# Optimization experiments

Measured on AMD Instinct MI355X. Metric: run time of the kernel, lower is better.

The kernel has to match this reference:

```python
import jax, jax.numpy as jnp
import numpy as np

N_NODES = 100000
N_EDGES = 1600000
IN_C = 128
OUT_C = 64
EDGE_DIM = 32
BN_EPS = 1e-5


def setup_inputs() -> dict:
    key = jax.random.key(0)
    ks = jax.random.split(key, 10)
    s = lambda fan_in: 1.0 / np.sqrt(fan_in)
    return {
        "x": jax.random.normal(ks[0], (N_NODES, IN_C), jnp.float32),
        "edge_index": jax.random.randint(ks[1], (2, N_EDGES), 0, N_NODES, jnp.int64),
        "edge_attr": jax.random.normal(ks[2], (N_EDGES, EDGE_DIM), jnp.float32),
        # SAGEConv params: lin_l (neighbors, with bias), lin_r (root, no bias)
        "W_l": jax.random.uniform(ks[3], (IN_C, OUT_C), jnp.float32, -s(IN_C), s(IN_C)),
        "b_l": jnp.zeros((OUT_C,), jnp.float32),
        "W_r": jax.random.uniform(ks[4], (IN_C, OUT_C), jnp.float32, -s(IN_C), s(IN_C)),
        # edge_transform: Linear(EDGE_DIM, OUT_C)
        "W_e": jax.random.uniform(ks[5], (EDGE_DIM, OUT_C), jnp.float32, -s(EDGE_DIM), s(EDGE_DIM)),
        "b_e": jax.random.uniform(ks[6], (OUT_C,), jnp.float32, -s(EDGE_DIM), s(EDGE_DIM)),
        # gate: Linear(2*OUT_C, OUT_C)
        "W_g": jax.random.uniform(ks[7], (2 * OUT_C, OUT_C), jnp.float32, -s(2 * OUT_C), s(2 * OUT_C)),
        "b_g": jax.random.uniform(ks[8], (OUT_C,), jnp.float32, -s(2 * OUT_C), s(2 * OUT_C)),
        # BatchNorm1d affine params
        "gamma": jnp.ones((OUT_C,), jnp.float32),
        "beta": jnp.zeros((OUT_C,), jnp.float32),
    }


def reference(x, edge_index, edge_attr, W_l, b_l, W_r, W_e, b_e, W_g, b_g, gamma, beta):
    n = x.shape[0]
    row, col = edge_index[0], edge_index[1]  # source, target

    # --- SAGEConv (mean aggregation): agg[i] = mean_{e: col[e]==i} x[row[e]]
    agg = jax.ops.segment_sum(x[row], col, num_segments=n)  # [N, IN_C]
    cnt = jax.ops.segment_sum(jnp.ones((row.shape[0],), x.dtype), col, num_segments=n)
    agg = agg / jnp.maximum(cnt, 1.0)[:, None]
    out = agg @ W_l + b_l + x @ W_r  # [N, OUT_C]

    # --- edge gating
    ea = edge_attr @ W_e + b_e  # [E, OUT_C]
    combined = jnp.concatenate([out[col], ea], axis=-1)  # [E, 2*OUT_C]
    gate = jax.nn.sigmoid(combined @ W_g + b_g)  # [E, OUT_C]
    contrib = gate * ea  # [E, OUT_C]
    out = out + jax.ops.segment_sum(contrib, col, num_segments=n)

    # --- BatchNorm1d (training: batch stats, biased variance)
    mu = jnp.mean(out, axis=0)
    var = jnp.mean(jnp.square(out - mu), axis=0)
    out = gamma * (out - mu) * jax.lax.rsqrt(var + BN_EPS) + beta

    # residual = Identity -> out + out, then ReLU
    return jax.nn.relu(2.0 * out)
```

## Files before the change

kernel.cpp:

```cpp
#include <hip/hip_runtime.h>
#include <math.h>

#define NN 100000
#define NE 1600000
#define INC 128
#define OC 64
#define ED 32

typedef __attribute__((ext_vector_type(8))) short bf16x8;
typedef __attribute__((ext_vector_type(4))) float f32x4;

__device__ __forceinline__ float sigmoidf_(float z) {
    return __builtin_amdgcn_rcpf(1.0f + __expf(-z));
}

__device__ __forceinline__ unsigned short f2bf(float x) {
    unsigned int u = __float_as_uint(x);
    unsigned int r = u + 0x7FFFu + ((u >> 16) & 1u);
    return (unsigned short)(r >> 16);
}
__device__ __forceinline__ float bf2f(unsigned short u) {
    return __uint_as_float((unsigned int)u << 16);
}
__device__ __forceinline__ unsigned cvtpk(float lo, float hi) {
    unsigned r;
    asm("v_cvt_pk_bf16_f32 %0, %1, %2" : "=v"(r) : "v"(lo), "v"(hi));
    return r;
}

extern "C" __global__ void __launch_bounds__(256)
k_wfuse(const float* __restrict__ We, const float* __restrict__ be,
        const float* __restrict__ Wg, const float* __restrict__ Wl,
        const float* __restrict__ Wr, unsigned short* __restrict__ WfT,
        unsigned short* __restrict__ WeT, float* __restrict__ hb,
        unsigned short* __restrict__ WlrT) {
    int idx = blockIdx.x * 256 + threadIdx.x;
    if (idx < ED * OC) {
        int ch = idx >> 5, d = idx & 31;
        float acc = 0.0f;
#pragma unroll
        for (int k = 0; k < OC; ++k)
            acc = fmaf(We[d * OC + k], Wg[(OC + k) * OC + ch], acc);
        WfT[idx] = f2bf(acc);
    } else if (idx < 2 * ED * OC) {
        int i2 = idx - ED * OC;
        int ch = i2 >> 5, d = i2 & 31;
        WeT[i2] = f2bf(We[d * OC + ch]);
    } else if (idx < 2 * ED * OC + OC) {
        int j = idx - 2 * ED * OC;
        float acc = 0.0f;
#pragma unroll
        for (int k = 0; k < OC; ++k)
            acc = fmaf(be[k], Wg[(OC + k) * OC + j], acc);
        hb[j] = acc;
    } else if (idx < 2 * ED * OC + OC + 2 * INC * OC) {
        int i3 = idx - (2 * ED * OC + OC);
        int ch = i3 >> 7, k = i3 & 127;
        float v = (ch < OC) ? Wl[k * OC + ch] : Wr[k * OC + (ch - OC)];
        WlrT[i3] = f2bf(v);
    }
}

extern "C" __global__ void __launch_bounds__(256)
k_xw(const float* __restrict__ x, const unsigned short* __restrict__ WlrT,
     unsigned short* __restrict__ ybf, unsigned short* __restrict__ xwrbf) {
    __shared__ unsigned short xs[64][136];
    int t = threadIdx.x;
    int base = blockIdx.x * 64;
    {
        int rr = t >> 2, cc = (t & 3) * 32;
        int grow = base + rr;
        if (grow < NN) {
            const float4* xp = reinterpret_cast<const float4*>(
                x + (size_t)grow * INC + cc);
#pragma unroll
            for (int q = 0; q < 8; ++q) {
                float4 v = xp[q];
                uint2 uv;
                uv.x = cvtpk(v.x, v.y);
                uv.y = cvtpk(v.z, v.w);
                *reinterpret_cast<uint2*>(&xs[rr][cc + q * 4]) = uv;
            }
        } else {
#pragma unroll
            for (int q = 0; q < 8; ++q) {
                uint2 uv; uv.x = 0u; uv.y = 0u;
                *reinterpret_cast<uint2*>(&xs[rr][cc + q * 4]) = uv;
            }
        }
    }
    __syncthreads();

    int lane = t & 63, w = t >> 6;
    int c = lane & 15, g = lane >> 4;

    bf16x8 bw0[4], bw1[4];
#pragma unroll
    for (int kk = 0; kk < 4; ++kk) {
        bw0[kk] = *reinterpret_cast<const bf16x8*>(
            WlrT + (w * 32 + 0 * 16 + c) * INC + kk * 32 + g * 8);
        bw1[kk] = *reinterpret_cast<const bf16x8*>(
            WlrT + (w * 32 + 1 * 16 + c) * INC + kk * 32 + g * 8);
    }

    f32x4 acc[4][2];
#pragma unroll
    for (int mt = 0; mt < 4; ++mt)
#pragma unroll
        for (int nt = 0; nt < 2; ++nt)
            acc[mt][nt] = (f32x4){0.0f, 0.0f, 0.0f, 0.0f};

#pragma unroll
    for (int kk = 0; kk < 4; ++kk) {
        bf16x8 a0 = *reinterpret_cast<const bf16x8*>(&xs[0 * 16 + c][kk * 32 + g * 8]);
        bf16x8 a1 = *reinterpret_cast<const bf16x8*>(&xs[1 * 16 + c][kk * 32 + g * 8]);
        bf16x8 a2 = *reinterpret_cast<const bf16x8*>(&xs[2 * 16 + c][kk * 32 + g * 8]);
        bf16x8 a3 = *reinterpret_cast<const bf16x8*>(&xs[3 * 16 + c][kk * 32 + g * 8]);
        acc[0][0] = __builtin_amdgcn_mfma_f32_16x16x32_bf16(a0, bw0[kk], acc[0][0], 0, 0, 0);
        acc[0][1] = __builtin_amdgcn_mfma_f32_16x16x32_bf16(a0, bw1[kk], acc[0][1], 0, 0, 0);
        acc[1][0] = __builtin_amdgcn_mfma_f32_16x16x32_bf16(a1, bw0[kk], acc[1][0], 0, 0, 0);
        acc[1][1] = __builtin_amdgcn_mfma_f32_16x16x32_bf16(a1, bw1[kk], acc[1][1], 0, 0, 0);
        acc[2][0] = __builtin_amdgcn_mfma_f32_16x16x32_bf16(a2, bw0[kk], acc[2][0], 0, 0, 0);
        acc[2][1] = __builtin_amdgcn_mfma_f32_16x16x32_bf16(a2, bw1[kk], acc[2][1], 0, 0, 0);
        acc[3][0] = __builtin_amdgcn_mfma_f32_16x16x32_bf16(a3, bw0[kk], acc[3][0], 0, 0, 0);
        acc[3][1] = __builtin_amdgcn_mfma_f32_16x16x32_bf16(a3, bw1[kk], acc[3][1], 0, 0, 0);
    }

#pragma unroll
    for (int mt = 0; mt < 4; ++mt) {
#pragma unroll
        for (int nt = 0; nt < 2; ++nt) {
            int ch = w * 32 + nt * 16 + c;
#pragma unroll
            for (int j = 0; j < 4; ++j) {
                int row = base + mt * 16 + g * 4 + j;
                if (row < NN) {
                    unsigned short vb = f2bf(acc[mt][nt][j]);
                    if (ch < OC) ybf[(size_t)row * OC + ch] = vb;
                    else         xwrbf[(size_t)row * OC + (ch - OC)] = vb;
                }
            }
        }
    }
}

extern "C" __global__ void __launch_bounds__(256)
k_hist(const int* __restrict__ colv, int* __restrict__ cnti) {
    int e = blockIdx.x * 256 + threadIdx.x;
    if (e >= NE) return;
    int cl = colv[e];
    cl = min(max(cl, 0), NN - 1);
    atomicAdd(&cnti[cl], 1);
}

extern "C" __global__ void __launch_bounds__(1024)
k_scanA(const int* __restrict__ cnti, int* __restrict__ cur,
        int* __restrict__ bsum) {
    __shared__ int s[1024];
    int t = threadIdx.x;
    int idx = blockIdx.x * 1024 + t;
    int v = (idx < NN) ? cnti[idx] : 0;
    s[t] = v;
    __syncthreads();
#pragma unroll
    for (int off = 1; off < 1024; off <<= 1) {
        int tmp = (t >= off) ? s[t - off] : 0;
        __syncthreads();
        s[t] += tmp;
        __syncthreads();
    }
    if (idx < NN) cur[idx] = s[t] - v;
    if (t == 1023) bsum[blockIdx.x] = s[1023];
}

extern "C" __global__ void __launch_bounds__(128)
k_scanB(int* __restrict__ bsum) {
    __shared__ int s[128];
    int t = threadIdx.x;
    int v = (t < 98) ? bsum[t] : 0;
    s[t] = v;
    __syncthreads();
#pragma unroll
    for (int off = 1; off < 128; off <<= 1) {
        int tmp = (t >= off) ? s[t - off] : 0;
        __syncthreads();
        s[t] += tmp;
        __syncthreads();
    }
    if (t < 98) bsum[t] = s[t] - v;
}

extern "C" __global__ void __launch_bounds__(1024)
k_scanC(int* __restrict__ cur, const int* __restrict__ bsum) {
    int idx = blockIdx.x * 1024 + threadIdx.x;
    if (idx < NN) cur[idx] += bsum[blockIdx.x];
}

extern "C" __global__ void __launch_bounds__(256)
k_bucket(const int* __restrict__ colv, const int* __restrict__ rowv,
         int* __restrict__ cur, unsigned long long* __restrict__ ec) {
    int e = blockIdx.x * 256 + threadIdx.x;
    if (e >= NE) return;
    int cl = colv[e];
    cl = min(max(cl, 0), NN - 1);
    int r = rowv[e];
    r = min(max(r, 0), NN - 1);
    int pos = atomicAdd(&cur[cl], 1);
    ec[pos] = ((unsigned long long)(unsigned)r << 47) |
              ((unsigned long long)(unsigned)cl << 30) | (unsigned)e;
}

extern "C" __global__ void __launch_bounds__(256)
k_aggoh(const unsigned long long* __restrict__ ec, const int* __restrict__ cur,
        const unsigned short* __restrict__ ybf, unsigned short* xwr_h,
        const float* __restrict__ bl, const float* __restrict__ Wg,
        const float* __restrict__ bg, const float* __restrict__ hb,
        float* __restrict__ agg) {
    __shared__ float ol[4][64];
    int w = threadIdx.x >> 6, c = threadIdx.x & 63;
    int i = blockIdx.x * 4 + w;
    if (i >= NN) return;
    int start = (i == 0) ? 0 : cur[i - 1];
    int end = cur[i];
    float xwr = bf2f(xwr_h[(size_t)i * OC + c]);
    float acc = 0.0f;
    int p = start;
    for (; p + 3 < end; p += 4) {
        int r0 = (int)(ec[p + 0] >> 47);
        int r1 = (int)(ec[p + 1] >> 47);
        int r2 = (int)(ec[p + 2] >> 47);
        int r3 = (int)(ec[p + 3] >> 47);
        unsigned short u0 = ybf[(size_t)r0 * OC + c];
        unsigned short u1 = ybf[(size_t)r1 * OC + c];
        unsigned short u2 = ybf[(size_t)r2 * OC + c];
        unsigned short u3 = ybf[(size_t)r3 * OC + c];
        acc += bf2f(u0);
        acc += bf2f(u1);
        acc += bf2f(u2);
        acc += bf2f(u3);
    }
    for (; p < end; ++p) {
        int r0 = (int)(ec[p] >> 47);
        acc += bf2f(ybf[(size_t)r0 * OC + c]);
    }
    float inv = 1.0f / fmaxf((float)(end - start), 1.0f);
    float o = fmaf(acc, inv, bl[c] + xwr);
    agg[(size_t)i * OC + c] = o;
    ol[w][c] = o;
    __builtin_amdgcn_wave_barrier();
    float h0 = bg[c] + hb[c];
    float h1 = 0.0f, h2 = 0.0f, h3 = 0.0f;
#pragma unroll
    for (int k = 0; k < OC; k += 4) {
        float o0 = ol[w][k + 0], o1 = ol[w][k + 1];
        float o2 = ol[w][k + 2], o3 = ol[w][k + 3];
        h0 = fmaf(o0, Wg[(k + 0) * OC + c], h0);
        h1 = fmaf(o1, Wg[(k + 1) * OC + c], h1);
        h2 = fmaf(o2, Wg[(k + 2) * OC + c], h2);
        h3 = fmaf(o3, Wg[(k + 3) * OC + c], h3);
    }
    float h = (h0 + h1) + (h2 + h3);
    xwr_h[(size_t)i * OC + (c & 15) * 4 + (c >> 4)] = f2bf(h);
}

extern "C" __global__ void __launch_bounds__(256, 3)
k_gate_ns(const unsigned long long* __restrict__ ec, const float* __restrict__ eattr,
          const unsigned short* __restrict__ WfT, const unsigned short* __restrict__ WeT,
          const float* __restrict__ be, const unsigned short* __restrict__ hswz,
          unsigned short* __restrict__ contrib) {
    int lane = threadIdx.x & 63;
    int w = threadIdx.x >> 6;
    int tb = (blockIdx.x * 4 + w) * 64;

    unsigned long long ev = ec[tb + lane];
    int e = (int)(ev & 0x3FFFFFFFULL);
    int cl = (int)((ev >> 30) & 0x1FFFFULL);
    int c = lane & 15, g = lane >> 4;

    int erow0 = __shfl(e, 0 * 16 + c);
    int erow1 = __shfl(e, 1 * 16 + c);
    int erow2 = __shfl(e, 2 * 16 + c);
    int erow3 = __shfl(e, 3 * 16 + c);
    int clx[16];
#pragma unroll
    for (int mt = 0; mt < 4; ++mt)
#pragma unroll
        for (int r = 0; r < 4; ++r)
            clx[mt * 4 + r] = __shfl(cl, mt * 16 + g * 4 + r);

    uint2 hg[16];
#pragma unroll
    for (int q = 0; q < 16; ++q)
        hg[q] = *reinterpret_cast<const uint2*>(hswz + (size_t)clx[q] * OC + c * 4);

    bf16x8 bwf[4], bwe[4];
    float bev[4];
#pragma unroll
    for (int nt = 0; nt < 4; ++nt) {
        int ch = nt * 16 + c;
        bwf[nt] = *reinterpret_cast<const bf16x8*>(WfT + ch * ED + g * 8);
        bwe[nt] = *reinterpret_cast<const bf16x8*>(WeT + ch * ED + g * 8);
        bev[nt] = be[ch];
    }

    float4 alo0 = reinterpret_cast<const float4*>(eattr + (size_t)erow0 * ED + g * 8)[0];
    float4 ahi0 = reinterpret_cast<const float4*>(eattr + (size_t)erow0 * ED + g * 8)[1];
    float4 alo1 = reinterpret_cast<const float4*>(eattr + (size_t)erow1 * ED + g * 8)[0];
    float4 ahi1 = reinterpret_cast<const float4*>(eattr + (size_t)erow1 * ED + g * 8)[1];
    float4 alo2 = reinterpret_cast<const float4*>(eattr + (size_t)erow2 * ED + g * 8)[0];
    float4 ahi2 = reinterpret_cast<const float4*>(eattr + (size_t)erow2 * ED + g * 8)[1];
    float4 alo3 = reinterpret_cast<const float4*>(eattr + (size_t)erow3 * ED + g * 8)[0];
    float4 ahi3 = reinterpret_cast<const float4*>(eattr + (size_t)erow3 * ED + g * 8)[1];

    bf16x8 afr[4];
    {
        union { bf16x8 v; unsigned d[4]; } pk;
#define PACKA(idx, lo, hi)                         \
        pk.d[0] = cvtpk(lo.x, lo.y);               \
        pk.d[1] = cvtpk(lo.z, lo.w);               \
        pk.d[2] = cvtpk(hi.x, hi.y);               \
        pk.d[3] = cvtpk(hi.z, hi.w);               \
        afr[idx] = pk.v;
        PACKA(0, alo0, ahi0)
        PACKA(1, alo1, ahi1)
        PACKA(2, alo2, ahi2)
        PACKA(3, alo3, ahi3)
#undef PACKA
    }

#pragma unroll
    for (int mt = 0; mt < 4; ++mt) {
        uint2 h0 = hg[mt * 4 + 0];
        uint2 h1 = hg[mt * 4 + 1];
        uint2 h2 = hg[mt * 4 + 2];
        uint2 h3 = hg[mt * 4 + 3];
        float sv[4][4];
#pragma unroll
        for (int nt = 0; nt < 4; ++nt) {
            f32x4 cz, ce;
            unsigned w0 = (nt < 2) ? h0.x : h0.y;
            unsigned w1 = (nt < 2) ? h1.x : h1.y;
            unsigned w2 = (nt < 2) ? h2.x : h2.y;
            unsigned w3 = (nt < 2) ? h3.x : h3.y;
            cz[0] = bf2f((unsigned short)((nt & 1) ? (w0 >> 16) : (w0 & 0xffffu)));
            cz[1] = bf2f((unsigned short)((nt & 1) ? (w1 >> 16) : (w1 & 0xffffu)));
            cz[2] = bf2f((unsigned short)((nt & 1) ? (w2 >> 16) : (w2 & 0xffffu)));
            cz[3] = bf2f((unsigned short)((nt & 1) ? (w3 >> 16) : (w3 & 0xffffu)));
            ce[0] = bev[nt]; ce[1] = bev[nt]; ce[2] = bev[nt]; ce[3] = bev[nt];
            f32x4 z  = __builtin_amdgcn_mfma_f32_16x16x32_bf16(afr[mt], bwf[nt], cz, 0, 0, 0);
            f32x4 ea = __builtin_amdgcn_mfma_f32_16x16x32_bf16(afr[mt], bwe[nt], ce, 0, 0, 0);
            sv[nt][0] = sigmoidf_(z[0]) * ea[0];
            sv[nt][1] = sigmoidf_(z[1]) * ea[1];
            sv[nt][2] = sigmoidf_(z[2]) * ea[2];
            sv[nt][3] = sigmoidf_(z[3]) * ea[3];
        }
#pragma unroll
        for (int r = 0; r < 4; ++r) {
            int row = tb + mt * 16 + g * 4 + r;
            uint2 pk;
            pk.x = cvtpk(sv[0][r], sv[1][r]);
            pk.y = cvtpk(sv[2][r], sv[3][r]);
            *reinterpret_cast<uint2*>(contrib + (size_t)row * OC + c * 4) = pk;
        }
    }
}

extern "C" __global__ void __launch_bounds__(256, 3)
k_gate_at(const unsigned long long* __restrict__ ec, const float* __restrict__ eattr,
          const unsigned short* __restrict__ WfT, const unsigned short* __restrict__ WeT,
          const float* __restrict__ be, const unsigned short* __restrict__ hswz,
          float* __restrict__ agg) {
    int lane = threadIdx.x & 63;
    int w = threadIdx.x >> 6;
    int tb = (blockIdx.x * 4 + w) * 64;

    unsigned long long ev = ec[tb + lane];
    int e = (int)(ev & 0x3FFFFFFFULL);
    int cl = (int)((ev >> 30) & 0x1FFFFULL);
    int c = lane & 15, g = lane >> 4;

    int erow0 = __shfl(e, 0 * 16 + c);
    int erow1 = __shfl(e, 1 * 16 + c);
    int erow2 = __shfl(e, 2 * 16 + c);
    int erow3 = __shfl(e, 3 * 16 + c);
    int clx[16];
#pragma unroll
    for (int mt = 0; mt < 4; ++mt)
#pragma unroll
        for (int r = 0; r < 4; ++r)
            clx[mt * 4 + r] = __shfl(cl, mt * 16 + g * 4 + r);

    uint2 hg[16];
#pragma unroll
    for (int q = 0; q < 16; ++q)
        hg[q] = *reinterpret_cast<const uint2*>(hswz + (size_t)clx[q] * OC + c * 4);

    bf16x8 bwf[4], bwe[4];
    float bev[4];
#pragma unroll
    for (int nt = 0; nt < 4; ++nt) {
        int ch = nt * 16 + c;
        bwf[nt] = *reinterpret_cast<const bf16x8*>(WfT + ch * ED + g * 8);
        bwe[nt] = *reinterpret_cast<const bf16x8*>(WeT + ch * ED + g * 8);
        bev[nt] = be[ch];
    }

    float4 alo0 = reinterpret_cast<const float4*>(eattr + (size_t)erow0 * ED + g * 8)[0];
    float4 ahi0 = reinterpret_cast<const float4*>(eattr + (size_t)erow0 * ED + g * 8)[1];
    float4 alo1 = reinterpret_cast<const float4*>(eattr + (size_t)erow1 * ED + g * 8)[0];
    float4 ahi1 = reinterpret_cast<const float4*>(eattr + (size_t)erow1 * ED + g * 8)[1];
    float4 alo2 = reinterpret_cast<const float4*>(eattr + (size_t)erow2 * ED + g * 8)[0];
    float4 ahi2 = reinterpret_cast<const float4*>(eattr + (size_t)erow2 * ED + g * 8)[1];
    float4 alo3 = reinterpret_cast<const float4*>(eattr + (size_t)erow3 * ED + g * 8)[0];
    float4 ahi3 = reinterpret_cast<const float4*>(eattr + (size_t)erow3 * ED + g * 8)[1];

    bf16x8 afr[4];
    {
        union { bf16x8 v; unsigned d[4]; } pk;
#define PACKA(idx, lo, hi)                         \
        pk.d[0] = cvtpk(lo.x, lo.y);               \
        pk.d[1] = cvtpk(lo.z, lo.w);               \
        pk.d[2] = cvtpk(hi.x, hi.y);               \
        pk.d[3] = cvtpk(hi.z, hi.w);               \
        afr[idx] = pk.v;
        PACKA(0, alo0, ahi0)
        PACKA(1, alo1, ahi1)
        PACKA(2, alo2, ahi2)
        PACKA(3, alo3, ahi3)
#undef PACKA
    }

#pragma unroll
    for (int mt = 0; mt < 4; ++mt) {
        int cl0 = clx[mt * 4 + 0];
        int cl1 = clx[mt * 4 + 1];
        int cl2 = clx[mt * 4 + 2];
        int cl3 = clx[mt * 4 + 3];
        uint2 h0 = hg[mt * 4 + 0];
        uint2 h1 = hg[mt * 4 + 1];
        uint2 h2 = hg[mt * 4 + 2];
        uint2 h3 = hg[mt * 4 + 3];
#pragma unroll
        for (int nt = 0; nt < 4; ++nt) {
            int ch = nt * 16 + c;
            f32x4 cz, ce;
            unsigned w0 = (nt < 2) ? h0.x : h0.y;
            unsigned w1 = (nt < 2) ? h1.x : h1.y;
            unsigned w2 = (nt < 2) ? h2.x : h2.y;
            unsigned w3 = (nt < 2) ? h3.x : h3.y;
            cz[0] = bf2f((unsigned short)((nt & 1) ? (w0 >> 16) : (w0 & 0xffffu)));
            cz[1] = bf2f((unsigned short)((nt & 1) ? (w1 >> 16) : (w1 & 0xffffu)));
            cz[2] = bf2f((unsigned short)((nt & 1) ? (w2 >> 16) : (w2 & 0xffffu)));
            cz[3] = bf2f((unsigned short)((nt & 1) ? (w3 >> 16) : (w3 & 0xffffu)));
            ce[0] = bev[nt]; ce[1] = bev[nt]; ce[2] = bev[nt]; ce[3] = bev[nt];
            f32x4 z  = __builtin_amdgcn_mfma_f32_16x16x32_bf16(afr[mt], bwf[nt], cz, 0, 0, 0);
            f32x4 ea = __builtin_amdgcn_mfma_f32_16x16x32_bf16(afr[mt], bwe[nt], ce, 0, 0, 0);
            float c0 = sigmoidf_(z[0]) * ea[0];
            float c1 = sigmoidf_(z[1]) * ea[1];
            float c2 = sigmoidf_(z[2]) * ea[2];
            float c3 = sigmoidf_(z[3]) * ea[3];
            float s = c0;
            int t = cl0;
            if (cl1 != t) { atomicAdd(&agg[(size_t)t * OC + ch], s); s = 0.0f; t = cl1; }
            s += c1;
            if (cl2 != t) { atomicAdd(&agg[(size_t)t * OC + ch], s); s = 0.0f; t = cl2; }
            s += c2;
            if (cl3 != t) { atomicAdd(&agg[(size_t)t * OC + ch], s); s = 0.0f; t = cl3; }
            s += c3;
            atomicAdd(&agg[(size_t)t * OC + ch], s);
        }
    }
}

extern "C" __global__ void __launch_bounds__(256)
k_csum(const unsigned short* __restrict__ contrib, const int* __restrict__ cur,
       float* __restrict__ agg) {
    int w = threadIdx.x >> 6, c = threadIdx.x & 63;
    int i = blockIdx.x * 4 + w;
    if (i >= NN) return;
    int start = (i == 0) ? 0 : cur[i - 1];
    int end = cur[i];
    float s = 0.0f;
    int p = start;
    for (; p + 3 < end; p += 4) {
        unsigned short u0 = contrib[(size_t)(p + 0) * OC + c];
        unsigned short u1 = contrib[(size_t)(p + 1) * OC + c];
        unsigned short u2 = contrib[(size_t)(p + 2) * OC + c];
        unsigned short u3 = contrib[(size_t)(p + 3) * OC + c];
        s += bf2f(u0);
        s += bf2f(u1);
        s += bf2f(u2);
        s += bf2f(u3);
    }
    for (; p < end; ++p) s += bf2f(contrib[(size_t)p * OC + c]);
    int ch = (c >> 2) + 16 * (c & 3);
    agg[(size_t)i * OC + ch] += s;
}

extern "C" __global__ void __launch_bounds__(256)
k_stats(const float* __restrict__ a, float* __restrict__ stats) {
    __shared__ float ls[256], lq[256];
    int t = threadIdx.x;
    float s = 0.0f, q = 0.0f;
    for (size_t idx = (size_t)blockIdx.x * 256 + t; idx < (size_t)NN * OC;
         idx += (size_t)gridDim.x * 256) {
        float v = a[idx];
        s += v;
        q = fmaf(v, v, q);
    }
    ls[t] = s; lq[t] = q;
    __syncthreads();
    if (t < OC) {
        s = ls[t] + ls[t + 64] + ls[t + 128] + ls[t + 192];
        q = lq[t] + lq[t + 64] + lq[t + 128] + lq[t + 192];
        atomicAdd(&stats[t], s);
        atomicAdd(&stats[OC + t], q);
    }
}

extern "C" __global__ void __launch_bounds__(256)
k_final(const float* __restrict__ a, const float* __restrict__ stats,
        const float* __restrict__ gamma, const float* __restrict__ beta,
        float* __restrict__ out) {
    size_t idx = (size_t)blockIdx.x * 256 + threadIdx.x;
    if (idx >= (size_t)NN * OC) return;
    int c = (int)(idx & 63);
    float mu = stats[c] * (1.0f / NN);
    float var = stats[OC + c] * (1.0f / NN) - mu * mu;
    float v = a[idx];
    float y = fmaf(gamma[c] * (v - mu), rsqrtf(var + 1e-5f), beta[c]);
    out[idx] = fmaxf(2.0f * y, 0.0f);
}

extern "C" void kernel_launch(void* const* d_in, const int* in_sizes, int n_in,
                              void* d_out, int out_size, void* d_ws, size_t ws_size,
                              hipStream_t stream) {
    const float* x     = (const float*)d_in[0];
    const int*   ei    = (const int*)d_in[1];
    const float* eattr = (const float*)d_in[2];
    const float* Wl    = (const float*)d_in[3];
    const float* bl    = (const float*)d_in[4];
    const float* Wr    = (const float*)d_in[5];
    const float* We    = (const float*)d_in[6];
    const float* be    = (const float*)d_in[7];
    const float* Wg    = (const float*)d_in[8];
    const float* bg    = (const float*)d_in[9];
    const float* gamma = (const float*)d_in[10];
    const float* beta  = (const float*)d_in[11];
    float* out = (float*)d_out;

    float* agg = (float*)d_ws;
    unsigned short* ybf   = (unsigned short*)(agg + (size_t)NN * OC);
    unsigned short* xwrbf = ybf + (size_t)NN * OC;
    unsigned long long* ec = (unsigned long long*)(xwrbf + (size_t)NN * OC);
    int* cur   = (int*)(ec + (size_t)NE);
    int* bsum  = cur + NN;
    float* stats = (float*)(bsum + 128);
    unsigned short* WfT  = (unsigned short*)(stats + 128);
    unsigned short* WeT  = WfT + ED * OC;
    unsigned short* WlrT = WeT + ED * OC;
    float* hb = (float*)(WlrT + 2 * INC * OC);
    unsigned short* contrib = (unsigned short*)(hb + OC);
    unsigned short* hswz = xwrbf;

    size_t base_bytes = (size_t)((char*)(hb + OC) - (char*)d_ws);
    bool ns = ws_size >= base_bytes + (size_t)NE * OC * sizeof(unsigned short);

    const int* rowv = ei;
    const int* colv = ei + NE;

    hipMemsetAsync(cur, 0, NN * sizeof(int), stream);
    hipMemsetAsync(stats, 0, 2 * OC * sizeof(float), stream);

    k_wfuse<<<(2 * ED * OC + OC + 2 * INC * OC + 255) / 256, 256, 0, stream>>>(
        We, be, Wg, Wl, Wr, WfT, WeT, hb, WlrT);
    k_xw<<<(NN + 63) / 64, 256, 0, stream>>>(x, WlrT, ybf, xwrbf);
    k_hist<<<(NE + 255) / 256, 256, 0, stream>>>(colv, cur);
    k_scanA<<<98, 1024, 0, stream>>>(cur, cur, bsum);
    k_scanB<<<1, 128, 0, stream>>>(bsum);
    k_scanC<<<98, 1024, 0, stream>>>(cur, bsum);
    k_bucket<<<(NE + 255) / 256, 256, 0, stream>>>(colv, rowv, cur, ec);
    k_aggoh<<<(NN + 3) / 4, 256, 0, stream>>>(ec, cur, ybf, xwrbf, bl, Wg, bg, hb, agg);
    if (ns) {
        k_gate_ns<<<NE / 256, 256, 0, stream>>>(ec, eattr, WfT, WeT, be, hswz, contrib);
        k_csum<<<(NN + 3) / 4, 256, 0, stream>>>(contrib, cur, agg);
    } else {
        k_gate_at<<<NE / 256, 256, 0, stream>>>(ec, eattr, WfT, WeT, be, hswz, agg);
    }
    k_stats<<<2048, 256, 0, stream>>>(agg, stats);
    k_final<<<((size_t)NN * OC + 255) / 256, 256, 0, stream>>>(agg, stats, gamma, beta, out);
}
```

Baseline: 557.3 us.

## Fuse histogram into xw GEMM, stats into csum, vectorize bucketing

The column histogram moves into the x·W kernel, and the standalone histogram launch is removed. The contribution-sum kernel now uses a grid-stride loop and also accumulates the BatchNorm sum and sum of squares, so the separate stats pass over agg is skipped on the non-atomic path. Bucketing now handles four edges per thread with int4 loads, and the neighbor-gather and csum loops are unrolled to eight. This cuts kernel launches and one full read of the activation matrix, at the cost of more atomics per thread and a different occupancy profile for the persistent csum grid.

```diff
diff --git a/kernel.cpp b/kernel.cpp
--- a/kernel.cpp
+++ b/kernel.cpp
@@ -63,9 +63,25 @@
 
 extern "C" __global__ void __launch_bounds__(256)
 k_xw(const float* __restrict__ x, const unsigned short* __restrict__ WlrT,
-     unsigned short* __restrict__ ybf, unsigned short* __restrict__ xwrbf) {
+     unsigned short* __restrict__ ybf, unsigned short* __restrict__ xwrbf,
+     const int* __restrict__ colv, int* __restrict__ cnti) {
+    int t = threadIdx.x;
+    {
+        int eb = (blockIdx.x * 256 + t) * 4;
+        if (eb + 3 < NE) {
+            int4 cv = *reinterpret_cast<const int4*>(colv + eb);
+            int c0 = min(max(cv.x, 0), NN - 1);
+            int c1 = min(max(cv.y, 0), NN - 1);
+            int c2 = min(max(cv.z, 0), NN - 1);
+            int c3 = min(max(cv.w, 0), NN - 1);
+            atomicAdd(&cnti[c0], 1);
+            atomicAdd(&cnti[c1], 1);
+            atomicAdd(&cnti[c2], 1);
+            atomicAdd(&cnti[c3], 1);
+        }
+    }
+
     __shared__ unsigned short xs[64][136];
-    int t = threadIdx.x;
     int base = blockIdx.x * 64;
     {
         int rr = t >> 2, cc = (t & 3) * 32;
@@ -144,15 +160,6 @@
     }
 }
 
-extern "C" __global__ void __launch_bounds__(256)
-k_hist(const int* __restrict__ colv, int* __restrict__ cnti) {
-    int e = blockIdx.x * 256 + threadIdx.x;
-    if (e >= NE) return;
-    int cl = colv[e];
-    cl = min(max(cl, 0), NN - 1);
-    atomicAdd(&cnti[cl], 1);
-}
-
 extern "C" __global__ void __launch_bounds__(1024)
 k_scanA(const int* __restrict__ cnti, int* __restrict__ cur,
         int* __restrict__ bsum) {
@@ -199,15 +206,26 @@
 extern "C" __global__ void __launch_bounds__(256)
 k_bucket(const int* __restrict__ colv, const int* __restrict__ rowv,
          int* __restrict__ cur, unsigned long long* __restrict__ ec) {
-    int e = blockIdx.x * 256 + threadIdx.x;
-    if (e >= NE) return;
-    int cl = colv[e];
-    cl = min(max(cl, 0), NN - 1);
-    int r = rowv[e];
-    r = min(max(r, 0), NN - 1);
-    int pos = atomicAdd(&cur[cl], 1);
-    ec[pos] = ((unsigned long long)(unsigned)r << 47) |
-              ((unsigned long long)(unsigned)cl << 30) | (unsigned)e;
+    int eb = (blockIdx.x * 256 + threadIdx.x) * 4;
+    if (eb >= NE) return;
+    int4 cv = *reinterpret_cast<const int4*>(colv + eb);
+    int4 rv = *reinterpret_cast<const int4*>(rowv + eb);
+    int c0 = min(max(cv.x, 0), NN - 1), r0 = min(max(rv.x, 0), NN - 1);
+    int c1 = min(max(cv.y, 0), NN - 1), r1 = min(max(rv.y, 0), NN - 1);
+    int c2 = min(max(cv.z, 0), NN - 1), r2 = min(max(rv.z, 0), NN - 1);
+    int c3 = min(max(cv.w, 0), NN - 1), r3 = min(max(rv.w, 0), NN - 1);
+    int p0 = atomicAdd(&cur[c0], 1);
+    int p1 = atomicAdd(&cur[c1], 1);
+    int p2 = atomicAdd(&cur[c2], 1);
+    int p3 = atomicAdd(&cur[c3], 1);
+    ec[p0] = ((unsigned long long)(unsigned)r0 << 47) |
+             ((unsigned long long)(unsigned)c0 << 30) | (unsigned)(eb + 0);
+    ec[p1] = ((unsigned long long)(unsigned)r1 << 47) |
+             ((unsigned long long)(unsigned)c1 << 30) | (unsigned)(eb + 1);
+    ec[p2] = ((unsigned long long)(unsigned)r2 << 47) |
+             ((unsigned long long)(unsigned)c2 << 30) | (unsigned)(eb + 2);
+    ec[p3] = ((unsigned long long)(unsigned)r3 << 47) |
+             ((unsigned long long)(unsigned)c3 << 30) | (unsigned)(eb + 3);
 }
 
 extern "C" __global__ void __launch_bounds__(256)
@@ -225,19 +243,25 @@
     float xwr = bf2f(xwr_h[(size_t)i * OC + c]);
     float acc = 0.0f;
     int p = start;
-    for (; p + 3 < end; p += 4) {
+    for (; p + 7 < end; p += 8) {
         int r0 = (int)(ec[p + 0] >> 47);
         int r1 = (int)(ec[p + 1] >> 47);
         int r2 = (int)(ec[p + 2] >> 47);
         int r3 = (int)(ec[p + 3] >> 47);
+        int r4 = (int)(ec[p + 4] >> 47);
+        int r5 = (int)(ec[p + 5] >> 47);
+        int r6 = (int)(ec[p + 6] >> 47);
+        int r7 = (int)(ec[p + 7] >> 47);
         unsigned short u0 = ybf[(size_t)r0 * OC + c];
         unsigned short u1 = ybf[(size_t)r1 * OC + c];
         unsigned short u2 = ybf[(size_t)r2 * OC + c];
         unsigned short u3 = ybf[(size_t)r3 * OC + c];
-        acc += bf2f(u0);
-        acc += bf2f(u1);
-        acc += bf2f(u2);
-        acc += bf2f(u3);
+        unsigned short u4 = ybf[(size_t)r4 * OC + c];
+        unsigned short u5 = ybf[(size_t)r5 * OC + c];
+        unsigned short u6 = ybf[(size_t)r6 * OC + c];
+        unsigned short u7 = ybf[(size_t)r7 * OC + c];
+        acc += bf2f(u0); acc += bf2f(u1); acc += bf2f(u2); acc += bf2f(u3);
+        acc += bf2f(u4); acc += bf2f(u5); acc += bf2f(u6); acc += bf2f(u7);
     }
     for (; p < end; ++p) {
         int r0 = (int)(ec[p] >> 47);
@@ -473,28 +497,44 @@
 }
 
 extern "C" __global__ void __launch_bounds__(256)
-k_csum(const unsigned short* __restrict__ contrib, const int* __restrict__ cur,
-       float* __restrict__ agg) {
+k_csumst(const unsigned short* __restrict__ contrib, const int* __restrict__ cur,
+         float* __restrict__ agg, float* __restrict__ stats) {
+    __shared__ float ls[256], lq[256];
     int w = threadIdx.x >> 6, c = threadIdx.x & 63;
-    int i = blockIdx.x * 4 + w;
-    if (i >= NN) return;
-    int start = (i == 0) ? 0 : cur[i - 1];
-    int end = cur[i];
-    float s = 0.0f;
-    int p = start;
-    for (; p + 3 < end; p += 4) {
-        unsigned short u0 = contrib[(size_t)(p + 0) * OC + c];
-        unsigned short u1 = contrib[(size_t)(p + 1) * OC + c];
-        unsigned short u2 = contrib[(size_t)(p + 2) * OC + c];
-        unsigned short u3 = contrib[(size_t)(p + 3) * OC + c];
-        s += bf2f(u0);
-        s += bf2f(u1);
-        s += bf2f(u2);
-        s += bf2f(u3);
-    }
-    for (; p < end; ++p) s += bf2f(contrib[(size_t)p * OC + c]);
     int ch = (c >> 2) + 16 * (c & 3);
-    agg[(size_t)i * OC + ch] += s;
+    float sv = 0.0f, sq = 0.0f;
+    for (int i = blockIdx.x * 4 + w; i < NN; i += 2048 * 4) {
+        int start = (i == 0) ? 0 : cur[i - 1];
+        int end = cur[i];
+        float s = 0.0f;
+        int p = start;
+        for (; p + 7 < end; p += 8) {
+            unsigned short u0 = contrib[(size_t)(p + 0) * OC + c];
+            unsigned short u1 = contrib[(size_t)(p + 1) * OC + c];
+            unsigned short u2 = contrib[(size_t)(p + 2) * OC + c];
+            unsigned short u3 = contrib[(size_t)(p + 3) * OC + c];
+            unsigned short u4 = contrib[(size_t)(p + 4) * OC + c];
+            unsigned short u5 = contrib[(size_t)(p + 5) * OC + c];
+            unsigned short u6 = contrib[(size_t)(p + 6) * OC + c];
+            unsigned short u7 = contrib[(size_t)(p + 7) * OC + c];
+            s += bf2f(u0); s += bf2f(u1); s += bf2f(u2); s += bf2f(u3);
+            s += bf2f(u4); s += bf2f(u5); s += bf2f(u6); s += bf2f(u7);
+        }
+        for (; p < end; ++p) s += bf2f(contrib[(size_t)p * OC + c]);
+        float v = agg[(size_t)i * OC + ch] + s;
+        agg[(size_t)i * OC + ch] = v;
+        sv += v;
+        sq = fmaf(v, v, sq);
+    }
+    ls[threadIdx.x] = sv;
+    lq[threadIdx.x] = sq;
+    __syncthreads();
+    if (threadIdx.x < 64) {
+        float a = ls[c] + ls[c + 64] + ls[c + 128] + ls[c + 192];
+        float b = lq[c] + lq[c + 64] + lq[c + 128] + lq[c + 192];
+        atomicAdd(&stats[ch], a);
+        atomicAdd(&stats[OC + ch], b);
+    }
 }
 
 extern "C" __global__ void __launch_bounds__(256)
@@ -574,19 +614,18 @@
 
     k_wfuse<<<(2 * ED * OC + OC + 2 * INC * OC + 255) / 256, 256, 0, stream>>>(
         We, be, Wg, Wl, Wr, WfT, WeT, hb, WlrT);
-    k_xw<<<(NN + 63) / 64, 256, 0, stream>>>(x, WlrT, ybf, xwrbf);
-    k_hist<<<(NE + 255) / 256, 256, 0, stream>>>(colv, cur);
+    k_xw<<<(NN + 63) / 64, 256, 0, stream>>>(x, WlrT, ybf, xwrbf, colv, cur);
     k_scanA<<<98, 1024, 0, stream>>>(cur, cur, bsum);
     k_scanB<<<1, 128, 0, stream>>>(bsum);
     k_scanC<<<98, 1024, 0, stream>>>(cur, bsum);
-    k_bucket<<<(NE + 255) / 256, 256, 0, stream>>>(colv, rowv, cur, ec);
+    k_bucket<<<(NE / 4 + 255) / 256, 256, 0, stream>>>(colv, rowv, cur, ec);
     k_aggoh<<<(NN + 3) / 4, 256, 0, stream>>>(ec, cur, ybf, xwrbf, bl, Wg, bg, hb, agg);
     if (ns) {
         k_gate_ns<<<NE / 256, 256, 0, stream>>>(ec, eattr, WfT, WeT, be, hswz, contrib);
-        k_csum<<<(NN + 3) / 4, 256, 0, stream>>>(contrib, cur, agg);
+        k_csumst<<<2048, 256, 0, stream>>>(contrib, cur, agg, stats);
     } else {
         k_gate_at<<<NE / 256, 256, 0, stream>>>(ec, eattr, WfT, WeT, be, hswz, agg);
-    }
-    k_stats<<<2048, 256, 0, stream>>>(agg, stats);
+        k_stats<<<2048, 256, 0, stream>>>(agg, stats);
+    }
     k_final<<<((size_t)NN * OC + 255) / 256, 256, 0, stream>>>(agg, stats, gamma, beta, out);
 }
```

After: 548.6 us. About the same (-1.6%).
